# Kernel tuning notes

Hardware: AMD Instinct MI355X
Metric: run time of the kernel (lower is better)

The kernel has to match this reference:

```python
import jax, jax.numpy as jnp
import numpy as np

E = 1024
H = 16
D = E // H  # head_dim = 64
B = 4
S = 2048


def setup_inputs() -> dict:
    key = jax.random.key(0)
    ks = jax.random.split(key, 10)
    sc = 1.0 / np.sqrt(E)
    return {
        "inputs": jax.random.normal(ks[0], (B, S, E), dtype=jnp.float32),
        "wq": jax.random.normal(ks[1], (E, E), dtype=jnp.float32) * sc,
        "bq": jnp.zeros((E,), dtype=jnp.float32),
        "wk": jax.random.normal(ks[2], (E, E), dtype=jnp.float32) * sc,
        "bk": jnp.zeros((E,), dtype=jnp.float32),
        "wv": jax.random.normal(ks[3], (E, E), dtype=jnp.float32) * sc,
        "bv": jnp.zeros((E,), dtype=jnp.float32),
        "wo": jax.random.normal(ks[4], (E, E), dtype=jnp.float32) * sc,
        "bo": jnp.zeros((E,), dtype=jnp.float32),
        "ln_gamma": jnp.ones((E,), dtype=jnp.float32),
        "ln_beta": jnp.zeros((E,), dtype=jnp.float32),
    }


def reference(inputs, wq, bq, wk, bk, wv, bv, wo, bo, ln_gamma, ln_beta):
    # QKV projections, split heads: [B,S,E] -> [B,H,S,D]
    def split_heads(x):
        return x.reshape(B, S, H, D).transpose(0, 2, 1, 3)

    q = split_heads(inputs @ wq + bq)
    k = split_heads(inputs @ wk + bk)
    v = split_heads(inputs @ wv + bv)

    scale = 1.0 / jnp.sqrt(jnp.asarray(D, dtype=inputs.dtype))
    score = jnp.einsum("bhqd,bhkd->bhqk", q, k) * scale  # [B,H,S,S]
    weights = jax.nn.softmax(score, axis=-1)
    out = jnp.einsum("bhqk,bhkd->bhqd", weights, v)  # [B,H,S,D]
    out = out.transpose(0, 2, 1, 3).reshape(B, S, E)
    out = out @ wo + bo

    # residual + LayerNorm(eps=1e-6)
    x = inputs + out
    mean = jnp.mean(x, axis=-1, keepdims=True)
    var = jnp.mean(jnp.square(x - mean), axis=-1, keepdims=True)
    x = (x - mean) * jax.lax.rsqrt(var + 1e-6)
    return x * ln_gamma + ln_beta
```

## Files before the change

kernel.cpp:

```cpp
#include <hip/hip_runtime.h>

#define E_DIM 1024
#define H_NUM 16
#define D_DIM 64
#define B_NUM 4
#define S_DIM 2048
#define M_DIM 8192

#define SCALE_Q 0.18033688011112042f
#define SMAX 10.0f

typedef _Float16 f16;
typedef __attribute__((ext_vector_type(4))) _Float16 f16x4;
typedef __attribute__((ext_vector_type(8))) _Float16 f16x8;
typedef __attribute__((ext_vector_type(2))) __fp16 h16x2;
typedef __attribute__((ext_vector_type(4))) float f32x4;

extern "C" __device__ float __ocml_native_exp2_f32(float);

#define MFMA32(a, b, c) __builtin_amdgcn_mfma_f32_16x16x32_f16(a, b, c, 0, 0, 0)

#define GLOBAL_LOAD_LDS_16(gp, lp)                                    \
  __builtin_amdgcn_global_load_lds(                                   \
      (const __attribute__((address_space(1))) void*)(gp),            \
      (__attribute__((address_space(3))) void*)(lp), 16, 0, 0)

__global__ __launch_bounds__(256) void k_prep(
    const float* __restrict__ x, f16* __restrict__ xh,
    const float* __restrict__ w0, const float* __restrict__ w1,
    const float* __restrict__ w2, const float* __restrict__ w3,
    f16* __restrict__ dst) {
  __shared__ float tile[32][33];
  if (blockIdx.x < 8192) {
    size_t i = ((size_t)blockIdx.x * 256 + threadIdx.x) * 4;
    float4 v = *reinterpret_cast<const float4*>(x + i);
    f16x4 o = {(f16)v.x, (f16)v.y, (f16)v.z, (f16)v.w};
    *reinterpret_cast<f16x4*>(xh + i) = o;
    return;
  }
  const int bid = blockIdx.x - 8192;
  const int z = bid >> 10;
  const int bx = (bid >> 5) & 31;
  const int by = bid & 31;
  const float* src = z == 0 ? w0 : z == 1 ? w1 : z == 2 ? w2 : w3;
  f16* out = dst + (size_t)z * (E_DIM * E_DIM);
  const int n0 = bx * 32, k0 = by * 32;
  const int tx = threadIdx.x & 31, ty = threadIdx.x >> 5;
#pragma unroll
  for (int i = 0; i < 4; i++)
    tile[ty + i * 8][tx] = src[(size_t)(k0 + ty + i * 8) * E_DIM + n0 + tx];
  __syncthreads();
#pragma unroll
  for (int i = 0; i < 4; i++)
    out[(size_t)(n0 + ty + i * 8) * E_DIM + k0 + tx] = (f16)tile[tx][ty + i * 8];
}


#define NKT (E_DIM / 64)
#define SLOT_A (256 * 64)
#define SLOT_B (128 * 64)
#define GEMM_LDS_BYTES (3 * (SLOT_A + SLOT_B) * 2)

__device__ __forceinline__ void gemm_mainloop_v4(
    const f16* __restrict__ A, const f16* __restrict__ BT,
    int m0, int n0, short* smem, f32x4 (&acc)[4][4]) {
  short* Asb = smem;
  short* Bsb = smem + 3 * SLOT_A;
  const int t = threadIdx.x;
  const int wave = t >> 6, lane = t & 63;
  const int l15 = lane & 15, quad = lane >> 4;
  const int wm = (wave >> 1) * 64, wn = (wave & 1) * 64;
  const int tr = t >> 3, tc = t & 7;
  const int swz = (tc ^ (tr & 7)) * 8;
  const int el = tc * 8;

  const f16* gA[4];
  const f16* gB[2];
  int eoA[4], eoB[2];
#pragma unroll
  for (int i = 0; i < 4; i++) {
    gA[i] = A + (size_t)(m0 + i * 64 + tr) * E_DIM + swz;
    eoA[i] = (i * 64 + tr) * 64 + el;
  }
#pragma unroll
  for (int j = 0; j < 2; j++) {
    gB[j] = BT + (size_t)(n0 + j * 64 + tr) * E_DIM + swz;
    eoB[j] = (j * 64 + tr) * 64 + el;
  }

  auto stage = [&](int slot, int kt) {
    short* ab = Asb + slot * SLOT_A;
    short* bb = Bsb + slot * SLOT_B;
    const int k0 = kt * 64;
#pragma unroll
    for (int i = 0; i < 4; i++) GLOBAL_LOAD_LDS_16(gA[i] + k0, ab + eoA[i]);
#pragma unroll
    for (int j = 0; j < 2; j++) GLOBAL_LOAD_LDS_16(gB[j] + k0, bb + eoB[j]);
  };

  stage(0, 0);
  stage(1, 1);
  stage(2, 2);

  for (int kt = 0; kt < NKT; kt++) {
    if (kt == 0)
      asm volatile("s_waitcnt vmcnt(12)" ::: "memory");
    else if (kt < NKT - 1)
      asm volatile("s_waitcnt vmcnt(6)" ::: "memory");
    else
      asm volatile("s_waitcnt vmcnt(0)" ::: "memory");
    __builtin_amdgcn_s_barrier();
    if (kt >= 1 && kt + 2 < NKT) stage((kt + 2) % 3, kt + 2);

    const short* as = Asb + (kt % 3) * SLOT_A;
    const short* bs = Bsb + (kt % 3) * SLOT_B;
    f16x8 af[4][2], bf[4][2];
#pragma unroll
    for (int mf = 0; mf < 4; mf++)
#pragma unroll
      for (int ks = 0; ks < 2; ks++)
        af[mf][ks] = *reinterpret_cast<const f16x8*>(
            &as[(wm + mf * 16 + l15) * 64 + ((ks * 4 + quad) ^ (l15 & 7)) * 8]);
#pragma unroll
    for (int nf = 0; nf < 4; nf++)
#pragma unroll
      for (int ks = 0; ks < 2; ks++)
        bf[nf][ks] = *reinterpret_cast<const f16x8*>(
            &bs[(wn + nf * 16 + l15) * 64 + ((ks * 4 + quad) ^ (l15 & 7)) * 8]);

    __builtin_amdgcn_s_setprio(1);
#pragma unroll
    for (int mf = 0; mf < 4; mf++)
#pragma unroll
      for (int nf = 0; nf < 4; nf++) {
        acc[mf][nf] = MFMA32(af[mf][0], bf[nf][0], acc[mf][nf]);
        acc[mf][nf] = MFMA32(af[mf][1], bf[nf][1], acc[mf][nf]);
      }
    __builtin_amdgcn_s_setprio(0);
    asm volatile("s_waitcnt lgkmcnt(0)" ::: "memory");
  }
}

__global__ __launch_bounds__(512, 2) void k_gemm_qkv_v4(
    const f16* __restrict__ A, const f16* __restrict__ BT3,
    const float* __restrict__ bq, const float* __restrict__ bk,
    const float* __restrict__ bv, f16* __restrict__ Qb,
    f16* __restrict__ Kb, f16* __restrict__ VT) {
  extern __shared__ short smem[];
  const int xcd = blockIdx.x & 7;
  const int s = blockIdx.x >> 3;
  const int sr = s >> 5;
  const int r5 = s & 31;
  const int yt = xcd * 4 + (r5 >> 3);
  const int xt = sr * 8 + (r5 & 7);
  const int m0 = yt * 256, n0 = xt * 128;
  const int region = xt >> 3;
  const float* bias = region == 0 ? bq : region == 1 ? bk : bv;
  const float scale = region == 0 ? SCALE_Q : 1.0f;

  f32x4 acc[4][4] = {};
  gemm_mainloop_v4(A, BT3, m0, n0, smem, acc);

  const int t = threadIdx.x;
  const int wave = t >> 6, lane = t & 63;
  const int l15 = lane & 15, quad = lane >> 4;
  const int wm = (wave >> 1) * 64, wn = (wave & 1) * 64;
#pragma unroll
  for (int nf = 0; nf < 4; nf++) {
    const int col = (n0 + wn + nf * 16 + l15) & 1023;
    const float bv_ = bias[col];
    const int hh = col >> 6, dd = col & 63;
#pragma unroll
    for (int mf = 0; mf < 4; mf++) {
#pragma unroll
      for (int r = 0; r < 4; r++) {
        const int row = m0 + wm + mf * 16 + quad * 4 + r;
        const f16 v = (f16)((acc[mf][nf][r] + bv_) * scale);
        if (region == 0) {
          Qb[(size_t)row * E_DIM + col] = v;
        } else if (region == 1) {
          Kb[(size_t)row * E_DIM + col] = v;
        } else {
          const int bb = row >> 11, ss = row & 2047;
          VT[(((size_t)bb * H_NUM + hh) * D_DIM + dd) * S_DIM + ss] = v;
        }
      }
    }
  }
}

__global__ __launch_bounds__(512, 2) void k_gemm_o_v4(
    const f16* __restrict__ A, const f16* __restrict__ BT,
    const float* __restrict__ bias, f16* __restrict__ Cout) {
  extern __shared__ short smem[];
  const int xcd = blockIdx.x & 7;
  const int s = blockIdx.x >> 3;
  const int yt = xcd * 4 + (s >> 3);
  const int xt = s & 7;
  const int m0 = yt * 256, n0 = xt * 128;

  f32x4 acc[4][4] = {};
  gemm_mainloop_v4(A, BT, m0, n0, smem, acc);

  const int t = threadIdx.x;
  const int wave = t >> 6, lane = t & 63;
  const int l15 = lane & 15, quad = lane >> 4;
  const int wm = (wave >> 1) * 64, wn = (wave & 1) * 64;
#pragma unroll
  for (int nf = 0; nf < 4; nf++) {
    const int col = n0 + wn + nf * 16 + l15;
    const float bv = bias[col];
#pragma unroll
    for (int mf = 0; mf < 4; mf++) {
#pragma unroll
      for (int r = 0; r < 4; r++) {
        const int row = m0 + wm + mf * 16 + quad * 4 + r;
        Cout[(size_t)row * E_DIM + col] = (f16)(acc[mf][nf][r] + bv);
      }
    }
  }
}

__global__ __launch_bounds__(256, 4) void k_attention(
    const f16* __restrict__ Q, const f16* __restrict__ K,
    const f16* __restrict__ VT, f16* __restrict__ O) {
  __shared__ short Ks[2][64 * 64];
  __shared__ short Vs[2][64 * 64];
  const int bh = blockIdx.x, qt = blockIdx.y;
  const int b = bh >> 4, h = bh & 15;
  const int t = threadIdx.x;
  const int wave = t >> 6, lane = t & 63, l15 = lane & 15, quad = lane >> 4;
  const size_t rowbase = (size_t)b * S_DIM;
  const int ch = h * D_DIM;
  const int qb = qt * 128 + wave * 32;

  f16x8 qf[2][2];
#pragma unroll
  for (int g = 0; g < 2; g++) {
    const size_t qrow = rowbase + qb + g * 16 + l15;
    qf[g][0] = *reinterpret_cast<const f16x8*>(Q + qrow * E_DIM + ch + quad * 8);
    qf[g][1] = *reinterpret_cast<const f16x8*>(Q + qrow * E_DIM + ch + 32 + quad * 8);
  }

  f32x4 o_acc[2][4] = {};
  f32x4 l_acc[2] = {};
  const f16x8 ones8 = {(f16)1.f, (f16)1.f, (f16)1.f, (f16)1.f,
                       (f16)1.f, (f16)1.f, (f16)1.f, (f16)1.f};
  const f32x4 cinit = {-SMAX, -SMAX, -SMAX, -SMAX};

  const int cgp = lane & 7;
  const f16* vtb = VT + ((size_t)(b * H_NUM + h) * D_DIM) * S_DIM;
  const f16* kgp[2];
  const f16* vgp[2];
  int ofs[2];
#pragma unroll
  for (int i = 0; i < 2; i++) {
    const int slot = wave * 16 + i * 8 + (lane >> 3);
    const int nt = slot >> 4, qd = (slot >> 2) & 3, rr = slot & 3;
    const int p = (nt >> 1) * 32 + qd * 8 + (nt & 1) * 4 + rr;
    const int cgl = (cgp ^ (slot & 7)) * 8;
    kgp[i] = K + (rowbase + p) * E_DIM + ch + cgl;
    vgp[i] = vtb + (size_t)slot * S_DIM + cgl;
    ofs[i] = slot * 64 + cgp * 8;
  }

  auto issue = [&](int bf) {
#pragma unroll
    for (int i = 0; i < 2; i++) {
      GLOBAL_LOAD_LDS_16(kgp[i], &Ks[bf][ofs[i]]);
      GLOBAL_LOAD_LDS_16(vgp[i], &Vs[bf][ofs[i]]);
      kgp[i] += 64 * E_DIM;
      vgp[i] += 64;
    }
  };

  issue(0);

  for (int kt = 0; kt < S_DIM / 64; kt++) {
    __syncthreads();
    if (kt + 1 < S_DIM / 64) issue((kt + 1) & 1);
    const short* kb = &Ks[kt & 1][0];
    const short* vb = &Vs[kt & 1][0];

    f32x4 sacc[2][4];
    __builtin_amdgcn_s_setprio(1);
#pragma unroll
    for (int nt = 0; nt < 4; nt++) {
      f16x8 kf0 = *reinterpret_cast<const f16x8*>(
          &kb[(nt * 16 + l15) * 64 + (quad ^ (l15 & 7)) * 8]);
      f16x8 kf1 = *reinterpret_cast<const f16x8*>(
          &kb[(nt * 16 + l15) * 64 + ((4 | quad) ^ (l15 & 7)) * 8]);
#pragma unroll
      for (int g = 0; g < 2; g++) {
        sacc[g][nt] = MFMA32(kf0, qf[g][0], cinit);
        sacc[g][nt] = MFMA32(kf1, qf[g][1], sacc[g][nt]);
      }
    }
    __builtin_amdgcn_s_setprio(0);

    f16x8 a8[2][2];
#pragma unroll
    for (int g = 0; g < 2; g++)
#pragma unroll
      for (int kk = 0; kk < 2; kk++) {
        union { f16x8 v8; h16x2 h2[4]; } u;
#pragma unroll
        for (int half = 0; half < 2; half++) {
          const f32x4 s4 = sacc[g][kk * 2 + half];
          u.h2[half * 2 + 0] = __builtin_amdgcn_cvt_pkrtz(
              __ocml_native_exp2_f32(s4[0]), __ocml_native_exp2_f32(s4[1]));
          u.h2[half * 2 + 1] = __builtin_amdgcn_cvt_pkrtz(
              __ocml_native_exp2_f32(s4[2]), __ocml_native_exp2_f32(s4[3]));
        }
        a8[g][kk] = u.v8;
      }

    __builtin_amdgcn_s_setprio(1);
#pragma unroll
    for (int kk = 0; kk < 2; kk++) {
#pragma unroll
      for (int dt = 0; dt < 4; dt++) {
        f16x8 vf = *reinterpret_cast<const f16x8*>(
            &vb[(dt * 16 + l15) * 64 + ((kk * 4 + quad) ^ (l15 & 7)) * 8]);
#pragma unroll
        for (int g = 0; g < 2; g++)
          o_acc[g][dt] = MFMA32(a8[g][kk], vf, o_acc[g][dt]);
      }
#pragma unroll
      for (int g = 0; g < 2; g++)
        l_acc[g] = MFMA32(a8[g][kk], ones8, l_acc[g]);
    }
    __builtin_amdgcn_s_setprio(0);
  }

#pragma unroll
  for (int g = 0; g < 2; g++) {
    const size_t obase = rowbase + qb + g * 16;
#pragma unroll
    for (int r = 0; r < 4; r++) {
      const float rl = 1.0f / l_acc[g][r];
#pragma unroll
      for (int dt = 0; dt < 4; dt++) {
        float v = o_acc[g][dt][r] * rl;
        O[(obase + quad * 4 + r) * E_DIM + ch + dt * 16 + l15] = (f16)v;
      }
    }
  }
}

__global__ __launch_bounds__(256) void k_ln(
    const f16* __restrict__ proj, const float* __restrict__ x,
    const float* __restrict__ gamma, const float* __restrict__ beta,
    float* __restrict__ out) {
  const int row = blockIdx.x;
  const int t = threadIdx.x;
  const size_t base = (size_t)row * E_DIM + t * 4;
  f16x4 p = *reinterpret_cast<const f16x4*>(proj + base);
  float4 xi = *reinterpret_cast<const float4*>(x + base);
  float v0 = (float)p[0] + xi.x, v1 = (float)p[1] + xi.y;
  float v2 = (float)p[2] + xi.z, v3 = (float)p[3] + xi.w;
  float s1 = v0 + v1 + v2 + v3;
  float s2 = v0 * v0 + v1 * v1 + v2 * v2 + v3 * v3;
#pragma unroll
  for (int off = 1; off < 64; off <<= 1) {
    s1 += __shfl_xor(s1, off, 64);
    s2 += __shfl_xor(s2, off, 64);
  }
  __shared__ float sh1[4], sh2[4];
  const int wave = t >> 6;
  if ((t & 63) == 0) { sh1[wave] = s1; sh2[wave] = s2; }
  __syncthreads();
  s1 = sh1[0] + sh1[1] + sh1[2] + sh1[3];
  s2 = sh2[0] + sh2[1] + sh2[2] + sh2[3];
  const float mean = s1 * (1.0f / E_DIM);
  const float var = s2 * (1.0f / E_DIM) - mean * mean;
  const float rstd = rsqrtf(var + 1e-6f);
  float4 g = *reinterpret_cast<const float4*>(gamma + t * 4);
  float4 bb = *reinterpret_cast<const float4*>(beta + t * 4);
  float4 o;
  o.x = (v0 - mean) * rstd * g.x + bb.x;
  o.y = (v1 - mean) * rstd * g.y + bb.y;
  o.z = (v2 - mean) * rstd * g.z + bb.z;
  o.w = (v3 - mean) * rstd * g.w + bb.w;
  *reinterpret_cast<float4*>(out + base) = o;
}

extern "C" void kernel_launch(void* const* d_in, const int* in_sizes, int n_in,
                              void* d_out, int out_size, void* d_ws, size_t ws_size,
                              hipStream_t stream) {
  const float* x     = (const float*)d_in[0];
  const float* wq    = (const float*)d_in[1];
  const float* bq    = (const float*)d_in[2];
  const float* wk    = (const float*)d_in[3];
  const float* bk    = (const float*)d_in[4];
  const float* wv    = (const float*)d_in[5];
  const float* bv    = (const float*)d_in[6];
  const float* wo    = (const float*)d_in[7];
  const float* bo    = (const float*)d_in[8];
  const float* gamma = (const float*)d_in[9];
  const float* beta  = (const float*)d_in[10];

  char* ws = (char*)d_ws;
  const size_t MB = 1ull << 20;
  f16* wt   = (f16*)(ws + 0 * MB);
  f16* wot  = (f16*)(ws + 6 * MB);
  f16* xh   = (f16*)(ws + 8 * MB);
  f16* Qb   = (f16*)(ws + 24 * MB);
  f16* Kb   = (f16*)(ws + 40 * MB);
  f16* VTb  = (f16*)(ws + 56 * MB);
  f16* Ob   = (f16*)(ws + 72 * MB);
  f16* proj = (f16*)(ws + 24 * MB);

  static int attr_set = 0;
  if (!attr_set) {
    hipFuncSetAttribute((const void*)k_gemm_qkv_v4,
                        hipFuncAttributeMaxDynamicSharedMemorySize, GEMM_LDS_BYTES);
    hipFuncSetAttribute((const void*)k_gemm_o_v4,
                        hipFuncAttributeMaxDynamicSharedMemorySize, GEMM_LDS_BYTES);
    attr_set = 1;
  }

  k_prep<<<12288, 256, 0, stream>>>(x, xh, wq, wk, wv, wo, wt);
  k_gemm_qkv_v4<<<768, 512, GEMM_LDS_BYTES, stream>>>(xh, wt, bq, bk, bv, Qb, Kb, VTb);
  k_attention<<<dim3(B_NUM * H_NUM, S_DIM / 128), 256, 0, stream>>>(Qb, Kb, VTb, Ob);
  k_gemm_o_v4<<<256, 512, GEMM_LDS_BYTES, stream>>>(Ob, wot, bo, proj);
  k_ln<<<M_DIM, 256, 0, stream>>>(proj, x, gamma, beta, (float*)d_out);
}
```

Baseline: 288.8 us.

## Shrink QKV GEMM K-step to 32 with packed-row swizzled LDS layout

The QKV projection GEMM mainloop now stages K-slices of 32 instead of 64. Two rows are packed per 64-element LDS line with an XOR swizzle, which cuts the triple-buffered LDS footprint from 144KB to 72KB, and launch bounds rise to 4 blocks per CU. The goal is higher occupancy so more waves can hide memory latency. The cost is twice as many barriers and waitcnt iterations per tile, each covering less MFMA work. The output GEMM keeps the old v4 mainloop.

```diff
diff --git a/kernel.cpp b/kernel.cpp
--- a/kernel.cpp
+++ b/kernel.cpp
@@ -56,92 +56,84 @@
 }
 
 
-#define NKT (E_DIM / 64)
-#define SLOT_A (256 * 64)
-#define SLOT_B (128 * 64)
-#define GEMM_LDS_BYTES (3 * (SLOT_A + SLOT_B) * 2)
-
-__device__ __forceinline__ void gemm_mainloop_v4(
+#define NU9 32
+#define UNIT9 12288
+#define QKV9_LDS_BYTES (3 * UNIT9 * 2)
+
+__device__ __forceinline__ void gemm_mainloop_v9(
     const f16* __restrict__ A, const f16* __restrict__ BT,
     int m0, int n0, short* smem, f32x4 (&acc)[4][4]) {
-  short* Asb = smem;
-  short* Bsb = smem + 3 * SLOT_A;
   const int t = threadIdx.x;
   const int wave = t >> 6, lane = t & 63;
   const int l15 = lane & 15, quad = lane >> 4;
   const int wm = (wave >> 1) * 64, wn = (wave & 1) * 64;
-  const int tr = t >> 3, tc = t & 7;
-  const int swz = (tc ^ (tr & 7)) * 8;
-  const int el = tc * 8;
-
-  const f16* gA[4];
-  const f16* gB[2];
-  int eoA[4], eoB[2];
-#pragma unroll
-  for (int i = 0; i < 4; i++) {
-    gA[i] = A + (size_t)(m0 + i * 64 + tr) * E_DIM + swz;
-    eoA[i] = (i * 64 + tr) * 64 + el;
-  }
-#pragma unroll
-  for (int j = 0; j < 2; j++) {
-    gB[j] = BT + (size_t)(n0 + j * 64 + tr) * E_DIM + swz;
-    eoB[j] = (j * 64 + tr) * 64 + el;
-  }
-
-  auto stage = [&](int slot, int kt) {
-    short* ab = Asb + slot * SLOT_A;
-    short* bb = Bsb + slot * SLOT_B;
-    const int k0 = kt * 64;
-#pragma unroll
-    for (int i = 0; i < 4; i++) GLOBAL_LOAD_LDS_16(gA[i] + k0, ab + eoA[i]);
-#pragma unroll
-    for (int j = 0; j < 2; j++) GLOBAL_LOAD_LDS_16(gB[j] + k0, bb + eoB[j]);
+
+  const f16* srcA[2];
+  int dofsA[2];
+#pragma unroll
+  for (int i = 0; i < 2; i++) {
+    const int p = (t >> 3) + i * 64;
+    const int v = (t & 7) ^ (p & 7);
+    const int r = 2 * p + (v >> 2);
+    const int kg = (v & 3) * 8;
+    srcA[i] = A + (size_t)(m0 + r) * E_DIM + kg;
+    dofsA[i] = t * 8 + i * 4096;
+  }
+  const int pB = t >> 3;
+  const int vB = (t & 7) ^ (pB & 7);
+  const int rB = 2 * pB + (vB >> 2);
+  const f16* srcB = BT + (size_t)(n0 + rB) * E_DIM + (vB & 3) * 8;
+  const int dofsB = t * 8;
+
+  auto stage = [&](int u) {
+    short* ab = smem + (u % 3) * UNIT9;
+    const int k0 = u * 32;
+    GLOBAL_LOAD_LDS_16(srcA[0] + k0, ab + dofsA[0]);
+    GLOBAL_LOAD_LDS_16(srcA[1] + k0, ab + dofsA[1]);
+    GLOBAL_LOAD_LDS_16(srcB + k0, ab + 8192 + dofsB);
   };
 
-  stage(0, 0);
-  stage(1, 1);
-  stage(2, 2);
-
-  for (int kt = 0; kt < NKT; kt++) {
+  stage(0); stage(1); stage(2);
+
+  for (int kt = 0; kt < NU9; kt++) {
     if (kt == 0)
-      asm volatile("s_waitcnt vmcnt(12)" ::: "memory");
-    else if (kt < NKT - 1)
       asm volatile("s_waitcnt vmcnt(6)" ::: "memory");
+    else if (kt < NU9 - 1)
+      asm volatile("s_waitcnt vmcnt(3)" ::: "memory");
     else
       asm volatile("s_waitcnt vmcnt(0)" ::: "memory");
     __builtin_amdgcn_s_barrier();
-    if (kt >= 1 && kt + 2 < NKT) stage((kt + 2) % 3, kt + 2);
-
-    const short* as = Asb + (kt % 3) * SLOT_A;
-    const short* bs = Bsb + (kt % 3) * SLOT_B;
-    f16x8 af[4][2], bf[4][2];
+    if (kt >= 1 && kt + 2 < NU9) stage(kt + 2);
+
+    const short* ub = smem + (kt % 3) * UNIT9;
+    f16x8 af[4], bf[4];
+#pragma unroll
+    for (int mf = 0; mf < 4; mf++) {
+      const int r = wm + mf * 16 + l15;
+      const int p = r >> 1;
+      af[mf] = *reinterpret_cast<const f16x8*>(
+          &ub[p * 64 + ((((r & 1) << 2) | quad) ^ (p & 7)) * 8]);
+    }
+#pragma unroll
+    for (int nf = 0; nf < 4; nf++) {
+      const int r = wn + nf * 16 + l15;
+      const int p = r >> 1;
+      bf[nf] = *reinterpret_cast<const f16x8*>(
+          &ub[8192 + p * 64 + ((((r & 1) << 2) | quad) ^ (p & 7)) * 8]);
+    }
+
+    __builtin_amdgcn_s_setprio(1);
 #pragma unroll
     for (int mf = 0; mf < 4; mf++)
 #pragma unroll
-      for (int ks = 0; ks < 2; ks++)
-        af[mf][ks] = *reinterpret_cast<const f16x8*>(
-            &as[(wm + mf * 16 + l15) * 64 + ((ks * 4 + quad) ^ (l15 & 7)) * 8]);
-#pragma unroll
-    for (int nf = 0; nf < 4; nf++)
-#pragma unroll
-      for (int ks = 0; ks < 2; ks++)
-        bf[nf][ks] = *reinterpret_cast<const f16x8*>(
-            &bs[(wn + nf * 16 + l15) * 64 + ((ks * 4 + quad) ^ (l15 & 7)) * 8]);
-
-    __builtin_amdgcn_s_setprio(1);
-#pragma unroll
-    for (int mf = 0; mf < 4; mf++)
-#pragma unroll
-      for (int nf = 0; nf < 4; nf++) {
-        acc[mf][nf] = MFMA32(af[mf][0], bf[nf][0], acc[mf][nf]);
-        acc[mf][nf] = MFMA32(af[mf][1], bf[nf][1], acc[mf][nf]);
-      }
+      for (int nf = 0; nf < 4; nf++)
+        acc[mf][nf] = MFMA32(af[mf], bf[nf], acc[mf][nf]);
     __builtin_amdgcn_s_setprio(0);
     asm volatile("s_waitcnt lgkmcnt(0)" ::: "memory");
   }
 }
 
-__global__ __launch_bounds__(512, 2) void k_gemm_qkv_v4(
+__global__ __launch_bounds__(512, 4) void k_gemm_qkv_v9(
     const f16* __restrict__ A, const f16* __restrict__ BT3,
     const float* __restrict__ bq, const float* __restrict__ bk,
     const float* __restrict__ bv, f16* __restrict__ Qb,
@@ -159,7 +151,7 @@
   const float scale = region == 0 ? SCALE_Q : 1.0f;
 
   f32x4 acc[4][4] = {};
-  gemm_mainloop_v4(A, BT3, m0, n0, smem, acc);
+  gemm_mainloop_v9(A, BT3, m0, n0, smem, acc);
 
   const int t = threadIdx.x;
   const int wave = t >> 6, lane = t & 63;
@@ -186,6 +178,92 @@
         }
       }
     }
+  }
+}
+
+
+#define NKT (E_DIM / 64)
+#define SLOT_A (256 * 64)
+#define SLOT_B (128 * 64)
+#define GEMM_LDS_BYTES (3 * (SLOT_A + SLOT_B) * 2)
+
+__device__ __forceinline__ void gemm_mainloop_v4(
+    const f16* __restrict__ A, const f16* __restrict__ BT,
+    int m0, int n0, short* smem, f32x4 (&acc)[4][4]) {
+  short* Asb = smem;
+  short* Bsb = smem + 3 * SLOT_A;
+  const int t = threadIdx.x;
+  const int wave = t >> 6, lane = t & 63;
+  const int l15 = lane & 15, quad = lane >> 4;
+  const int wm = (wave >> 1) * 64, wn = (wave & 1) * 64;
+  const int tr = t >> 3, tc = t & 7;
+  const int swz = (tc ^ (tr & 7)) * 8;
+  const int el = tc * 8;
+
+  const f16* gA[4];
+  const f16* gB[2];
+  int eoA[4], eoB[2];
+#pragma unroll
+  for (int i = 0; i < 4; i++) {
+    gA[i] = A + (size_t)(m0 + i * 64 + tr) * E_DIM + swz;
+    eoA[i] = (i * 64 + tr) * 64 + el;
+  }
+#pragma unroll
+  for (int j = 0; j < 2; j++) {
+    gB[j] = BT + (size_t)(n0 + j * 64 + tr) * E_DIM + swz;
+    eoB[j] = (j * 64 + tr) * 64 + el;
+  }
+
+  auto stage = [&](int slot, int kt) {
+    short* ab = Asb + slot * SLOT_A;
+    short* bb = Bsb + slot * SLOT_B;
+    const int k0 = kt * 64;
+#pragma unroll
+    for (int i = 0; i < 4; i++) GLOBAL_LOAD_LDS_16(gA[i] + k0, ab + eoA[i]);
+#pragma unroll
+    for (int j = 0; j < 2; j++) GLOBAL_LOAD_LDS_16(gB[j] + k0, bb + eoB[j]);
+  };
+
+  stage(0, 0);
+  stage(1, 1);
+  stage(2, 2);
+
+  for (int kt = 0; kt < NKT; kt++) {
+    if (kt == 0)
+      asm volatile("s_waitcnt vmcnt(12)" ::: "memory");
+    else if (kt < NKT - 1)
+      asm volatile("s_waitcnt vmcnt(6)" ::: "memory");
+    else
+      asm volatile("s_waitcnt vmcnt(0)" ::: "memory");
+    __builtin_amdgcn_s_barrier();
+    if (kt >= 1 && kt + 2 < NKT) stage((kt + 2) % 3, kt + 2);
+
+    const short* as = Asb + (kt % 3) * SLOT_A;
+    const short* bs = Bsb + (kt % 3) * SLOT_B;
+    f16x8 af[4][2], bf[4][2];
+#pragma unroll
+    for (int mf = 0; mf < 4; mf++)
+#pragma unroll
+      for (int ks = 0; ks < 2; ks++)
+        af[mf][ks] = *reinterpret_cast<const f16x8*>(
+            &as[(wm + mf * 16 + l15) * 64 + ((ks * 4 + quad) ^ (l15 & 7)) * 8]);
+#pragma unroll
+    for (int nf = 0; nf < 4; nf++)
+#pragma unroll
+      for (int ks = 0; ks < 2; ks++)
+        bf[nf][ks] = *reinterpret_cast<const f16x8*>(
+            &bs[(wn + nf * 16 + l15) * 64 + ((ks * 4 + quad) ^ (l15 & 7)) * 8]);
+
+    __builtin_amdgcn_s_setprio(1);
+#pragma unroll
+    for (int mf = 0; mf < 4; mf++)
+#pragma unroll
+      for (int nf = 0; nf < 4; nf++) {
+        acc[mf][nf] = MFMA32(af[mf][0], bf[nf][0], acc[mf][nf]);
+        acc[mf][nf] = MFMA32(af[mf][1], bf[nf][1], acc[mf][nf]);
+      }
+    __builtin_amdgcn_s_setprio(0);
+    asm volatile("s_waitcnt lgkmcnt(0)" ::: "memory");
   }
 }
 
@@ -413,15 +491,15 @@
 
   static int attr_set = 0;
   if (!attr_set) {
-    hipFuncSetAttribute((const void*)k_gemm_qkv_v4,
-                        hipFuncAttributeMaxDynamicSharedMemorySize, GEMM_LDS_BYTES);
+    hipFuncSetAttribute((const void*)k_gemm_qkv_v9,
+                        hipFuncAttributeMaxDynamicSharedMemorySize, QKV9_LDS_BYTES);
     hipFuncSetAttribute((const void*)k_gemm_o_v4,
                         hipFuncAttributeMaxDynamicSharedMemorySize, GEMM_LDS_BYTES);
     attr_set = 1;
   }
 
   k_prep<<<12288, 256, 0, stream>>>(x, xh, wq, wk, wv, wo, wt);
-  k_gemm_qkv_v4<<<768, 512, GEMM_LDS_BYTES, stream>>>(xh, wt, bq, bk, bv, Qb, Kb, VTb);
+  k_gemm_qkv_v9<<<768, 512, QKV9_LDS_BYTES, stream>>>(xh, wt, bq, bk, bv, Qb, Kb, VTb);
   k_attention<<<dim3(B_NUM * H_NUM, S_DIM / 128), 256, 0, stream>>>(Qb, Kb, VTb, Ob);
   k_gemm_o_v4<<<256, 512, GEMM_LDS_BYTES, stream>>>(Ob, wot, bo, proj);
   k_ln<<<M_DIM, 256, 0, stream>>>(proj, x, gamma, beta, (float*)d_out);
```

New measurement: 284.7 us. About the same (-1.4%).
